# Optimization experiments

Measured on AMD Instinct MI355X. Metric: run time of the kernel, lower is better.

Reference implementation:

```python
import jax, jax.numpy as jnp
import numpy as np

N_NODES = 100000
N_EDGES = 1600000
IN_DIM = 256
OUT_DIM = 128


def setup_inputs() -> dict:
    key = jax.random.key(0)
    k1, k2, k3, k4, k5, k6 = jax.random.split(key, 6)
    H = jax.random.normal(k1, (N_NODES, IN_DIM), dtype=jnp.float32)
    std = 1.0 / np.sqrt(OUT_DIM)
    weight = jax.random.uniform(k2, (IN_DIM, OUT_DIM), dtype=jnp.float32, minval=-std, maxval=std)
    bias = jax.random.uniform(k3, (OUT_DIM,), dtype=jnp.float32, minval=-std, maxval=std)
    # COO representation of the normalized sparse adjacency A [N, N]
    src = jax.random.randint(k4, (N_EDGES,), 0, N_NODES, dtype=jnp.int32)
    dst = jnp.sort(jax.random.randint(k5, (N_EDGES,), 0, N_NODES, dtype=jnp.int32))
    vals = jax.random.uniform(k6, (N_EDGES,), dtype=jnp.float32) / 16.0  # ~row-normalized
    return {"H": H, "weight": weight, "bias": bias, "vals": vals, "src": src, "dst": dst}


def reference(H, weight, bias, vals, src, dst):
    # Dense transform: [N, K] @ [K, D] -> [N, D]
    HW = H @ weight
    # SpMM (A @ HW) as gather-scale-scatter over COO edges
    msg = HW[src] * vals[:, None]                      # [E, D]
    out = jax.ops.segment_sum(msg, dst, num_segments=H.shape[0])
    return out + bias
```

## Files before the change

kernel.cpp:

```cpp
#include <hip/hip_runtime.h>
#include <hip/hip_bf16.h>

#define N_NODES 100000
#define N_EDGES 1600000
#define IN_DIM 256
#define OUT_DIM 128

typedef __attribute__((ext_vector_type(4))) float f32x4;
typedef __attribute__((ext_vector_type(8))) short s16x8;

__device__ inline unsigned short f2bf_us(float f) {
    union { __hip_bfloat16 h; unsigned short u; } v;
    v.h = __float2bfloat16(f);
    return v.u;
}

__device__ inline s16x8 pack8(const float4& a, const float4& b) {
    union { s16x8 v; __hip_bfloat162 h[4]; } u;
    u.h[0] = __float22bfloat162_rn(make_float2(a.x, a.y));
    u.h[1] = __float22bfloat162_rn(make_float2(a.z, a.w));
    u.h[2] = __float22bfloat162_rn(make_float2(b.x, b.y));
    u.h[3] = __float22bfloat162_rn(make_float2(b.z, b.w));
    return u.v;
}

__global__ __launch_bounds__(256)
void wt_kernel(const float* __restrict__ W, unsigned short* __restrict__ WTx) {
    const int t = blockIdx.x * 256 + threadIdx.x;
    const int j    = t & 7;
    const int lrow = (t >> 3) & 15;
    const int kblk = (t >> 7) & 3;
    const int kc   = (t >> 9) & 7;
    const int n    = t >> 12;
    const int k    = kc * 32 + kblk * 8 + j;
    const int c    = n * 16 + lrow;
    WTx[t] = f2bf_us(W[(size_t)k * OUT_DIM + c]);
}

__global__ __launch_bounds__(256, 2)
void gemm_mfma_kernel(const float* __restrict__ H,
                      const unsigned short* __restrict__ WTx,
                      unsigned short* __restrict__ HWb) {
    const int tid  = threadIdx.x;
    const int wid  = tid >> 6;
    const int lane = tid & 63;
    const int lrow = lane & 15;
    const int kblk = lane >> 4;
    const int wrow = blockIdx.x * 128 + wid * 32;

    int r0 = wrow + lrow;       if (r0 >= N_NODES) r0 = N_NODES - 1;
    int r1 = wrow + lrow + 16;  if (r1 >= N_NODES) r1 = N_NODES - 1;
    const float* p0 = H + (size_t)r0 * IN_DIM + kblk * 8;
    const float* p1 = H + (size_t)r1 * IN_DIM + kblk * 8;

    const unsigned short* wbase = WTx + (size_t)(kblk * 16 + lrow) * 8;

    f32x4 acc[2][8] = {};

    float4 c00 = *(const float4*)(p0);
    float4 c01 = *(const float4*)(p0 + 4);
    float4 c10 = *(const float4*)(p1);
    float4 c11 = *(const float4*)(p1 + 4);

    #pragma unroll
    for (int kc = 0; kc < 8; ++kc) {
        const s16x8 fa0 = pack8(c00, c01);
        const s16x8 fa1 = pack8(c10, c11);
        if (kc < 7) {
            const float* q0 = p0 + (kc + 1) * 32;
            const float* q1 = p1 + (kc + 1) * 32;
            c00 = *(const float4*)(q0);
            c01 = *(const float4*)(q0 + 4);
            c10 = *(const float4*)(q1);
            c11 = *(const float4*)(q1 + 4);
        }
        #pragma unroll
        for (int n = 0; n < 8; ++n) {
            const s16x8 fb = *(const s16x8*)(wbase + ((size_t)(n * 8 + kc) << 9));
            acc[0][n] = __builtin_amdgcn_mfma_f32_16x16x32_bf16(fa0, fb, acc[0][n], 0, 0, 0);
            acc[1][n] = __builtin_amdgcn_mfma_f32_16x16x32_bf16(fa1, fb, acc[1][n], 0, 0, 0);
        }
    }

    #pragma unroll
    for (int mt = 0; mt < 2; ++mt) {
        #pragma unroll
        for (int r = 0; r < 4; ++r) {
            const int grow = wrow + mt * 16 + (lane >> 4) * 4 + r;
            if (grow < N_NODES) {
                #pragma unroll
                for (int n = 0; n < 8; ++n)
                    HWb[(size_t)grow * OUT_DIM + n * 16 + (lane & 15)] =
                        f2bf_us(acc[mt][n][r]);
            }
        }
    }
}

__global__ __launch_bounds__(256)
void rowptr_kernel(const int* __restrict__ dst, int* __restrict__ row_ptr) {
    const int e = blockIdx.x * blockDim.x + threadIdx.x;
    if (e > N_EDGES) return;
    if (e == N_EDGES) {
        for (int n = dst[N_EDGES - 1] + 1; n <= N_NODES; ++n) row_ptr[n] = N_EDGES;
        return;
    }
    const int d = dst[e];
    const int dprev = (e == 0) ? -1 : dst[e - 1];
    for (int n = dprev + 1; n <= d; ++n) row_ptr[n] = e;
}

__global__ __launch_bounds__(256)
void spmm_v3_kernel(const uint4* __restrict__ HWq, const float* __restrict__ vals,
                    const int* __restrict__ src, const int* __restrict__ row_ptr,
                    const float* __restrict__ bias, float* __restrict__ out) {
    const int node = blockIdx.x * 4 + (threadIdx.x >> 6);
    if (node >= N_NODES) return;
    const int lane  = threadIdx.x & 63;
    const int eslot = lane >> 4;
    const int cg    = lane & 15;

    const int lo = row_ptr[node];
    const int hi = row_ptr[node + 1];

    float acc[8] = {};
    for (int base = lo; base < hi; base += 8) {
        const int e0 = base + eslot;
        const int e1 = base + 4 + eslot;
        const bool m0 = e0 < hi;
        const bool m1 = e1 < hi;
        const int ec0 = m0 ? e0 : lo;
        const int ec1 = m1 ? e1 : lo;
        const int   s0 = src[ec0];
        const int   s1 = src[ec1];
        const float v0 = m0 ? vals[ec0] : 0.f;
        const float v1 = m1 ? vals[ec1] : 0.f;
        const uint4 g0 = HWq[(size_t)s0 * 16 + cg];
        const uint4 g1 = HWq[(size_t)s1 * 16 + cg];

        const unsigned* u0 = (const unsigned*)&g0;
        const unsigned* u1 = (const unsigned*)&g1;
        #pragma unroll
        for (int j = 0; j < 4; ++j) {
            acc[2*j]   = fmaf(__uint_as_float(u0[j] << 16),         v0, acc[2*j]);
            acc[2*j+1] = fmaf(__uint_as_float(u0[j] & 0xffff0000u), v0, acc[2*j+1]);
        }
        #pragma unroll
        for (int j = 0; j < 4; ++j) {
            acc[2*j]   = fmaf(__uint_as_float(u1[j] << 16),         v1, acc[2*j]);
            acc[2*j+1] = fmaf(__uint_as_float(u1[j] & 0xffff0000u), v1, acc[2*j+1]);
        }
    }

    #pragma unroll
    for (int i = 0; i < 8; ++i) {
        acc[i] += __shfl_xor(acc[i], 16);
        acc[i] += __shfl_xor(acc[i], 32);
    }

    if (lane < 16) {
        float4 o0, o1;
        const float* bb = bias + cg * 8;
        o0.x = acc[0] + bb[0]; o0.y = acc[1] + bb[1];
        o0.z = acc[2] + bb[2]; o0.w = acc[3] + bb[3];
        o1.x = acc[4] + bb[4]; o1.y = acc[5] + bb[5];
        o1.z = acc[6] + bb[6]; o1.w = acc[7] + bb[7];
        float* p = out + (size_t)node * OUT_DIM + cg * 8;
        *(float4*)(p)     = o0;
        *(float4*)(p + 4) = o1;
    }
}

extern "C" void kernel_launch(void* const* d_in, const int* in_sizes, int n_in,
                              void* d_out, int out_size, void* d_ws, size_t ws_size,
                              hipStream_t stream) {
    const float* H    = (const float*)d_in[0];
    const float* W    = (const float*)d_in[1];
    const float* bias = (const float*)d_in[2];
    const float* vals = (const float*)d_in[3];
    const int*   src  = (const int*)d_in[4];
    const int*   dst  = (const int*)d_in[5];
    float* out = (float*)d_out;

    unsigned short* HWb = (unsigned short*)d_ws;
    const size_t hw_bytes = (size_t)N_NODES * OUT_DIM * sizeof(unsigned short);
    int* row_ptr = (int*)((char*)d_ws + hw_bytes);
    size_t wt_off = hw_bytes + (size_t)(N_NODES + 1) * sizeof(int);
    wt_off = (wt_off + 127) & ~(size_t)127;
    unsigned short* WTx = (unsigned short*)((char*)d_ws + wt_off);

    wt_kernel<<<dim3((IN_DIM * OUT_DIM) / 256), dim3(256), 0, stream>>>(W, WTx);
    rowptr_kernel<<<dim3((N_EDGES + 256) / 256), dim3(256), 0, stream>>>(dst, row_ptr);
    gemm_mfma_kernel<<<dim3((N_NODES + 127) / 128), dim3(256), 0, stream>>>(H, WTx, HWb);
    spmm_v3_kernel<<<dim3((N_NODES + 3) / 4), dim3(256), 0, stream>>>(
        (const uint4*)HWb, vals, src, row_ptr, bias, out);
}
```

Measured before the change: 121.2 us.

## Stage H tiles into LDS via async global_load_lds with double buffering

```diff
diff --git a/kernel.cpp b/kernel.cpp
--- a/kernel.cpp
+++ b/kernel.cpp
@@ -22,6 +22,12 @@
     u.h[2] = __float22bfloat162_rn(make_float2(b.x, b.y));
     u.h[3] = __float22bfloat162_rn(make_float2(b.z, b.w));
     return u.v;
+}
+
+__device__ inline void gload_lds16(const float* g, float* l) {
+    __builtin_amdgcn_global_load_lds(
+        (const __attribute__((address_space(1))) unsigned*)g,
+        (__attribute__((address_space(3))) unsigned*)l, 16, 0, 0);
 }
 
 __global__ __launch_bounds__(256)
@@ -37,61 +43,73 @@
     WTx[t] = f2bf_us(W[(size_t)k * OUT_DIM + c]);
 }
 
-__global__ __launch_bounds__(256, 2)
+__global__ __launch_bounds__(256, 3)
 void gemm_mfma_kernel(const float* __restrict__ H,
                       const unsigned short* __restrict__ WTx,
-                      unsigned short* __restrict__ HWb) {
+                      unsigned short* __restrict__ HWp) {
+    __shared__ float Hs[2][4096];
+
     const int tid  = threadIdx.x;
     const int wid  = tid >> 6;
     const int lane = tid & 63;
     const int lrow = lane & 15;
     const int kblk = lane >> 4;
-    const int wrow = blockIdx.x * 128 + wid * 32;
-
-    int r0 = wrow + lrow;       if (r0 >= N_NODES) r0 = N_NODES - 1;
-    int r1 = wrow + lrow + 16;  if (r1 >= N_NODES) r1 = N_NODES - 1;
-    const float* p0 = H + (size_t)r0 * IN_DIM + kblk * 8;
-    const float* p1 = H + (size_t)r1 * IN_DIM + kblk * 8;
+    const int brow = blockIdx.x * 128;
 
     const unsigned short* wbase = WTx + (size_t)(kblk * 16 + lrow) * 8;
 
     f32x4 acc[2][8] = {};
 
-    float4 c00 = *(const float4*)(p0);
-    float4 c01 = *(const float4*)(p0 + 4);
-    float4 c10 = *(const float4*)(p1);
-    float4 c11 = *(const float4*)(p1 + 4);
-
-    #pragma unroll
+    auto stage = [&](int b, int kc) {
+        #pragma unroll
+        for (int i = 0; i < 4; ++i) {
+            const int ubase = i * 256 + wid * 64;
+            const int unit  = ubase + lane;
+            const int row   = unit >> 3;
+            const int ul    = (unit & 7) ^ (row & 7);
+            int grow = brow + row; if (grow >= N_NODES) grow = N_NODES - 1;
+            const float* gsrc = H + (size_t)grow * IN_DIM + kc * 32 + ul * 4;
+            gload_lds16(gsrc, &Hs[b][ubase * 4]);
+        }
+    };
+
+    stage(0, 0);
+    __syncthreads();
+
     for (int kc = 0; kc < 8; ++kc) {
-        const s16x8 fa0 = pack8(c00, c01);
-        const s16x8 fa1 = pack8(c10, c11);
-        if (kc < 7) {
-            const float* q0 = p0 + (kc + 1) * 32;
-            const float* q1 = p1 + (kc + 1) * 32;
-            c00 = *(const float4*)(q0);
-            c01 = *(const float4*)(q0 + 4);
-            c10 = *(const float4*)(q1);
-            c11 = *(const float4*)(q1 + 4);
+        const int cur = kc & 1;
+        if (kc < 7) stage(cur ^ 1, kc + 1);
+
+        s16x8 fa[2];
+        #pragma unroll
+        for (int mt = 0; mt < 2; ++mt) {
+            const int row = wid * 32 + mt * 16 + lrow;
+            const int u0  = (kblk * 2) ^ (row & 7);
+            const int u1  = (kblk * 2 + 1) ^ (row & 7);
+            const float4 x0 = *(const float4*)&Hs[cur][(row * 8 + u0) * 4];
+            const float4 x1 = *(const float4*)&Hs[cur][(row * 8 + u1) * 4];
+            fa[mt] = pack8(x0, x1);
         }
         #pragma unroll
         for (int n = 0; n < 8; ++n) {
             const s16x8 fb = *(const s16x8*)(wbase + ((size_t)(n * 8 + kc) << 9));
-            acc[0][n] = __builtin_amdgcn_mfma_f32_16x16x32_bf16(fa0, fb, acc[0][n], 0, 0, 0);
-            acc[1][n] = __builtin_amdgcn_mfma_f32_16x16x32_bf16(fa1, fb, acc[1][n], 0, 0, 0);
-        }
-    }
-
+            acc[0][n] = __builtin_amdgcn_mfma_f32_16x16x32_bf16(fa[0], fb, acc[0][n], 0, 0, 0);
+            acc[1][n] = __builtin_amdgcn_mfma_f32_16x16x32_bf16(fa[1], fb, acc[1][n], 0, 0, 0);
+        }
+        __syncthreads();
+    }
+
+    const int c = lane & 15;
     #pragma unroll
     for (int mt = 0; mt < 2; ++mt) {
         #pragma unroll
         for (int r = 0; r < 4; ++r) {
-            const int grow = wrow + mt * 16 + (lane >> 4) * 4 + r;
+            const int grow = brow + wid * 32 + mt * 16 + (lane >> 4) * 4 + r;
             if (grow < N_NODES) {
+                unsigned short tmp[8];
                 #pragma unroll
-                for (int n = 0; n < 8; ++n)
-                    HWb[(size_t)grow * OUT_DIM + n * 16 + (lane & 15)] =
-                        f2bf_us(acc[mt][n][r]);
+                for (int n = 0; n < 8; ++n) tmp[n] = f2bf_us(acc[mt][n][r]);
+                *(s16x8*)(HWp + (size_t)grow * OUT_DIM + c * 8) = *(const s16x8*)tmp;
             }
         }
     }
@@ -159,15 +177,9 @@
     }
 
     if (lane < 16) {
-        float4 o0, o1;
-        const float* bb = bias + cg * 8;
-        o0.x = acc[0] + bb[0]; o0.y = acc[1] + bb[1];
-        o0.z = acc[2] + bb[2]; o0.w = acc[3] + bb[3];
-        o1.x = acc[4] + bb[4]; o1.y = acc[5] + bb[5];
-        o1.z = acc[6] + bb[6]; o1.w = acc[7] + bb[7];
-        float* p = out + (size_t)node * OUT_DIM + cg * 8;
-        *(float4*)(p)     = o0;
-        *(float4*)(p + 4) = o1;
+        #pragma unroll
+        for (int j = 0; j < 8; ++j)
+            out[(size_t)node * OUT_DIM + j * 16 + cg] = acc[j] + bias[j * 16 + cg];
     }
 }
 
@@ -182,7 +194,7 @@
     const int*   dst  = (const int*)d_in[5];
     float* out = (float*)d_out;
 
-    unsigned short* HWb = (unsigned short*)d_ws;
+    unsigned short* HWp = (unsigned short*)d_ws;
     const size_t hw_bytes = (size_t)N_NODES * OUT_DIM * sizeof(unsigned short);
     int* row_ptr = (int*)((char*)d_ws + hw_bytes);
     size_t wt_off = hw_bytes + (size_t)(N_NODES + 1) * sizeof(int);
@@ -191,7 +203,7 @@
 
     wt_kernel<<<dim3((IN_DIM * OUT_DIM) / 256), dim3(256), 0, stream>>>(W, WTx);
     rowptr_kernel<<<dim3((N_EDGES + 256) / 256), dim3(256), 0, stream>>>(dst, row_ptr);
-    gemm_mfma_kernel<<<dim3((N_NODES + 127) / 128), dim3(256), 0, stream>>>(H, WTx, HWb);
+    gemm_mfma_kernel<<<dim3((N_NODES + 127) / 128), dim3(256), 0, stream>>>(H, WTx, HWp);
     spmm_v3_kernel<<<dim3((N_NODES + 3) / 4), dim3(256), 0, stream>>>(
-        (const uint4*)HWb, vals, src, row_ptr, bias, out);
-}
+        (const uint4*)HWp, vals, src, row_ptr, bias, out);
+}
```

After: 105.4 us. -13.0%, faster.
